# Performance work log

Measured on AMD Instinct MI355X. Metric: run time of the kernel, lower is better.

Reference implementation:

```python
import jax, jax.numpy as jnp
import numpy as np
import math

N, T, D = 4096, 32, 158
NEWS, DGRU = 1024, 128
G, E, H, K = 8, 8, 4, 2          # groups, experts/group, heads, top_k
HID = G * E                       # 64
DH = E // H                       # head_dim = 2
NEG = -1e30


def setup_inputs() -> dict:
    key = jax.random.key(0)
    ks = jax.random.split(key, 16)
    s = 0.05
    price_feature = jax.random.normal(ks[0], (N, T, D), jnp.float32)
    news_feature = jax.random.normal(ks[1], (N, T, NEWS), jnp.float32)
    news_mask = jax.random.uniform(ks[2], (N, T), dtype=jnp.float32)
    # simple deterministic router params (stand-in for injected router module)
    router_W = jax.random.normal(ks[3], (D + NEWS, DGRU), jnp.float32) * s
    router_b = jnp.zeros((DGRU,), jnp.float32)
    # hidden_to_gate: Linear(d_gru -> hidden_dim)
    gate_W = jax.random.normal(ks[4], (DGRU, HID), jnp.float32) * s
    gate_b = jnp.zeros((HID,), jnp.float32)
    # 64 tiny experts: Linear(hidden_dim -> 1), stacked [G,E,HID]
    expert_W = jax.random.normal(ks[5], (G, E, HID), jnp.float32) * s
    expert_b = jnp.zeros((G, E), jnp.float32)
    # per-group attention weights, torch Linear layout [out,in] -> [G,E,E]
    wq = jax.random.normal(ks[6], (G, E, E), jnp.float32) * s
    wk = jax.random.normal(ks[7], (G, E, E), jnp.float32) * s
    wv = jax.random.normal(ks[8], (G, E, E), jnp.float32) * s
    wo = jax.random.normal(ks[9], (G, E, E), jnp.float32) * s
    wq_b = jnp.zeros((G, E), jnp.float32)
    wk_b = jnp.zeros((G, E), jnp.float32)
    wv_b = jnp.zeros((G, E), jnp.float32)
    wo_b = jnp.zeros((G, E), jnp.float32)
    return dict(price_feature=price_feature, news_feature=news_feature, news_mask=news_mask,
                router_W=router_W, router_b=router_b, gate_W=gate_W, gate_b=gate_b,
                expert_W=expert_W, expert_b=expert_b,
                wq=wq, wq_b=wq_b, wk=wk, wk_b=wk_b, wv=wv, wv_b=wv_b, wo=wo, wo_b=wo_b)


def _forward(price_feature, news_feature, news_mask, router_W, router_b,
             gate_W, gate_b, expert_W, expert_b,
             wq, wq_b, wk, wk_b, wv, wv_b, wo, wo_b):
    n = price_feature.shape[0]
    # ---- router: masked temporal pooling + linear + tanh -> [N, d_gru]
    m = news_mask[:, :, None]
    news_agg = (news_feature * m).sum(1) / jnp.clip(m.sum(1), 1e-6)
    price_agg = price_feature.mean(1)
    h = jnp.tanh(jnp.concatenate([price_agg, news_agg], axis=-1) @ router_W + router_b)
    # ---- gate: [N, HID]
    hidden = h @ gate_W + gate_b
    # ---- top-k routing with scatter mask + masked softmax
    top_k_values, top_k_indices = jax.lax.top_k(hidden, K)
    mask = jnp.zeros_like(hidden).at[jnp.arange(n)[:, None], top_k_indices].set(1.0)
    masked_hidden = jnp.where(mask == 0, NEG, hidden)
    routing_weights = jax.nn.softmax(masked_hidden, axis=1)  # [N, HID]
    # ---- all 64 experts at once: [N, G, E]
    expert_out = jnp.einsum('nh,geh->nge', hidden, expert_W) + expert_b
    # ---- inner-group attention (faithful to torch view/transpose layout)
    q = jnp.einsum('nge,gfe->ngf', expert_out, wq) + wq_b
    k = jnp.einsum('nge,gfe->ngf', expert_out, wk) + wk_b
    v = jnp.einsum('nge,gfe->ngf', expert_out, wv) + wv_b
    # view [N,G,H,DH] then transpose(1,2) -> attend over DH positions, H as features
    qt = q.reshape(n, G, H, DH).transpose(0, 1, 3, 2)  # [N,G,DH,H]
    kt = k.reshape(n, G, H, DH).transpose(0, 1, 3, 2)
    vt = v.reshape(n, G, H, DH).transpose(0, 1, 3, 2)
    scores = jnp.einsum('ngdh,ngeh->ngde', qt, kt) / math.sqrt(DH)  # [N,G,DH,DH]
    attn = jax.nn.softmax(scores, axis=-1)
    attended = jnp.einsum('ngde,ngeh->ngdh', attn, vt)  # [N,G,DH,H]
    attended = attended.transpose(0, 1, 3, 2).reshape(n, G, E)
    agg = jnp.einsum('nge,gfe->ngf', attended, wo) + wo_b  # [N,G,E]
    all_outputs = agg.reshape(n, HID)
    weighted = all_outputs * routing_weights
    predictions = weighted.sum(axis=1)  # [N]
    return predictions, routing_weights, hidden, top_k_indices, routing_weights


def reference(price_feature, news_feature, news_mask, router_W, router_b,
              gate_W, gate_b, expert_W, expert_b,
              wq, wq_b, wk, wk_b, wv, wv_b, wo, wo_b):
    return _forward(price_feature, news_feature, news_mask, router_W, router_b,
                    gate_W, gate_b, expert_W, expert_b,
                    wq, wq_b, wk, wk_b, wv, wv_b, wo, wo_b)
```

## Files before the change

kernel.cpp:

```cpp
#include <hip/hip_runtime.h>
#include <math.h>

namespace {

constexpr int TT    = 32;
constexpr int DD    = 158;
constexpr int NEWSC = 1024;
constexpr int XPAD  = 1184;
constexpr int NOFF  = 160;
constexpr int DGRU  = 128;
constexpr int HIDN  = 64;
constexpr int RPB   = 8;

__global__ __launch_bounds__(256)
void agg_kernel(const float* __restrict__ price,
                const float* __restrict__ news,
                const float* __restrict__ mask,
                float* __restrict__ x)
{
  const int r   = blockIdx.x;
  const int tid = threadIdx.x;
  __shared__ float m_s[TT];

  if (tid < TT) m_s[tid] = mask[(size_t)r * TT + tid];
  __syncthreads();

  float den = 0.f;
  #pragma unroll
  for (int t = 0; t < TT; ++t) den += m_s[t];
  den = fmaxf(den, 1e-6f);
  const float rden = 1.0f / den;

  {
    const int j0 = tid * 4;
    const float* nb = news + (size_t)r * TT * NEWSC + j0;
    float ax = 0.f, ay = 0.f, az = 0.f, aw = 0.f;
    #pragma unroll
    for (int t = 0; t < TT; ++t) {
      const float  mv = m_s[t];
      const float4 nv = *(const float4*)(nb + (size_t)t * NEWSC);
      ax += mv * nv.x; ay += mv * nv.y; az += mv * nv.z; aw += mv * nv.w;
    }
    float4 o4 = make_float4(ax * rden, ay * rden, az * rden, aw * rden);
    *(float4*)(x + (size_t)r * XPAD + NOFF + j0) = o4;
  }

  if (tid < DD) {
    const float* pr = price + (size_t)r * TT * DD + tid;
    float acc = 0.f;
    #pragma unroll
    for (int t = 0; t < TT; ++t) acc += pr[(size_t)t * DD];
    x[(size_t)r * XPAD + tid] = acc * (1.0f / (float)TT);
  }
}

__global__ __launch_bounds__(256)
void moe_kernel(const float* __restrict__ x,
                const float* __restrict__ rW,
                const float* __restrict__ rb,
                const float* __restrict__ gW,
                const float* __restrict__ gb,
                const float* __restrict__ eW,
                const float* __restrict__ eb,
                const float* __restrict__ wq,
                const float* __restrict__ wqb,
                const float* __restrict__ wk,
                const float* __restrict__ wkb,
                const float* __restrict__ wv,
                const float* __restrict__ wvb,
                const float* __restrict__ wo,
                const float* __restrict__ wob,
                float* __restrict__ out, int nrows)
{
  __shared__ float hs[RPB][DGRU];
  __shared__ float part[RPB][DGRU];
  __shared__ float hid_s[RPB][HIDN];
  __shared__ float eo_s[RPB][HIDN];
  __shared__ float q_s[RPB][HIDN];
  __shared__ float k_s[RPB][HIDN];
  __shared__ float v_s[RPB][HIDN];
  __shared__ float att_s[RPB][HIDN];

  const int tid  = threadIdx.x;
  const int row0 = blockIdx.x * RPB;

  {
    const int sh = tid >> 7;
    const int o  = tid & 127;
    float acc[RPB];
    #pragma unroll
    for (int r = 0; r < RPB; ++r) acc[r] = 0.f;

    const float* xb = x + (size_t)row0 * XPAD;

    auto seg = [&](int b, int e, int xbase, int wbase) {
      int i = b;
      for (; i + 8 <= e; i += 8) {
        float w[8];
        #pragma unroll
        for (int kk = 0; kk < 8; ++kk)
          w[kk] = rW[(size_t)(wbase + i + kk) * DGRU + o];
        #pragma unroll
        for (int r = 0; r < RPB; ++r) {
          const float* xr = xb + (size_t)r * XPAD + xbase + i;
          acc[r] += xr[0] * w[0] + xr[1] * w[1] + xr[2] * w[2] + xr[3] * w[3]
                  + xr[4] * w[4] + xr[5] * w[5] + xr[6] * w[6] + xr[7] * w[7];
        }
      }
      for (; i < e; ++i) {
        const float w = rW[(size_t)(wbase + i) * DGRU + o];
        #pragma unroll
        for (int r = 0; r < RPB; ++r)
          acc[r] += xb[(size_t)r * XPAD + xbase + i] * w;
      }
    };

    if (!sh) {
      seg(0, 80, 0, 0);
      seg(0, 512, NOFF, DD);
    } else {
      seg(80, DD, 0, 0);
      seg(512, NEWSC, NOFF, DD);
    }

    if (sh) {
      #pragma unroll
      for (int r = 0; r < RPB; ++r) part[r][o] = acc[r];
    }
    __syncthreads();
    if (!sh) {
      const float b = rb[o];
      #pragma unroll
      for (int r = 0; r < RPB; ++r) hs[r][o] = tanhf(acc[r] + part[r][o] + b);
    }
  }
  __syncthreads();

  const int wgi = tid >> 6;
  const int ln  = tid & 63;
  const int ra  = wgi;
  const int rb2 = wgi + 4;

  float h0 = gb[ln], h1 = gb[ln];
  #pragma unroll 4
  for (int i = 0; i < DGRU; ++i) {
    const float w = gW[(size_t)i * HIDN + ln];
    h0 += hs[ra][i]  * w;
    h1 += hs[rb2][i] * w;
  }
  hid_s[ra][ln]  = h0;
  hid_s[rb2][ln] = h1;
  __syncthreads();

  float* out_pred = out;
  float* out_rw1  = out + (size_t)nrows;
  float* out_hid  = out + (size_t)nrows * 65;
  float* out_idx  = out + (size_t)nrows * 129;
  float* out_rw2  = out + (size_t)nrows * 131;

  const float hvv[2] = {h0, h1};
  int   i1v[2], i2v[2];
  float w1v[2], w2v[2];
  #pragma unroll
  for (int rr = 0; rr < 2; ++rr) {
    const int r   = wgi + rr * 4;
    const int row = row0 + r;
    const float hv = hvv[rr];
    float bv = hv; int bi = ln;
    #pragma unroll
    for (int off = 32; off >= 1; off >>= 1) {
      const float ov = __shfl_xor(bv, off);
      const int   oi = __shfl_xor(bi, off);
      if (ov > bv || (ov == bv && oi < bi)) { bv = ov; bi = oi; }
    }
    float cv = (ln == bi) ? -1e30f : hv; int ci = ln;
    #pragma unroll
    for (int off = 32; off >= 1; off >>= 1) {
      const float ov = __shfl_xor(cv, off);
      const int   oi = __shfl_xor(ci, off);
      if (ov > cv || (ov == cv && oi < ci)) { cv = ov; ci = oi; }
    }
    const float e2 = expf(cv - bv);
    const float zi = 1.0f / (1.0f + e2);
    const float rwl = (ln == bi) ? zi : (ln == ci) ? e2 * zi : 0.0f;
    out_hid[(size_t)row * 64 + ln] = hv;
    out_rw1[(size_t)row * 64 + ln] = rwl;
    out_rw2[(size_t)row * 64 + ln] = rwl;
    if (ln < 2) out_idx[(size_t)row * 2 + ln] = (float)(ln == 0 ? bi : ci);
    i1v[rr] = bi; i2v[rr] = ci; w1v[rr] = zi; w2v[rr] = e2 * zi;
  }

  {
    float a0 = eb[ln], a1 = eb[ln];
    const float4* ew4 = (const float4*)(eW + (size_t)ln * HIDN);
    #pragma unroll
    for (int c = 0; c < 16; ++c) {
      const float4 w4 = ew4[c];
      const int j = c * 4;
      a0 += hid_s[ra][j]  * w4.x + hid_s[ra][j+1]  * w4.y
          + hid_s[ra][j+2]  * w4.z + hid_s[ra][j+3]  * w4.w;
      a1 += hid_s[rb2][j] * w4.x + hid_s[rb2][j+1] * w4.y
          + hid_s[rb2][j+2] * w4.z + hid_s[rb2][j+3] * w4.w;
    }
    eo_s[ra][ln]  = a0;
    eo_s[rb2][ln] = a1;
  }
  __syncthreads();

  const int gg = ln >> 3;
  #pragma unroll
  for (int rr = 0; rr < 2; ++rr) {
    const int r = wgi + rr * 4;
    float aq = wqb[ln], ak = wkb[ln], av = wvb[ln];
    #pragma unroll
    for (int ee = 0; ee < 8; ++ee) {
      const float xv = eo_s[r][gg * 8 + ee];
      aq += xv * wq[ln * 8 + ee];
      ak += xv * wk[ln * 8 + ee];
      av += xv * wv[ln * 8 + ee];
    }
    q_s[r][ln] = aq; k_s[r][ln] = ak; v_s[r][ln] = av;
  }
  __syncthreads();

  {
    const int e8  = ln & 7;
    const int dd2 = e8 & 1;
    const int hh  = e8 >> 1;
    const float rs2 = 0.7071067811865476f;
    #pragma unroll
    for (int rr = 0; rr < 2; ++rr) {
      const int r = wgi + rr * 4;
      float s0 = 0.f, s1 = 0.f;
      #pragma unroll
      for (int h2 = 0; h2 < 4; ++h2) {
        const float qv = q_s[r][gg * 8 + h2 * 2 + dd2];
        s0 += qv * k_s[r][gg * 8 + h2 * 2 + 0];
        s1 += qv * k_s[r][gg * 8 + h2 * 2 + 1];
      }
      s0 *= rs2; s1 *= rs2;
      const float mx = fmaxf(s0, s1);
      const float a0 = expf(s0 - mx);
      const float a1 = expf(s1 - mx);
      const float zi = 1.0f / (a0 + a1);
      att_s[r][ln] = (a0 * v_s[r][gg * 8 + hh * 2 + 0]
                    + a1 * v_s[r][gg * 8 + hh * 2 + 1]) * zi;
    }
  }
  __syncthreads();

  #pragma unroll
  for (int rr = 0; rr < 2; ++rr) {
    const int r   = wgi + rr * 4;
    const int row = row0 + r;
    float acc = wob[ln];
    #pragma unroll
    for (int ee = 0; ee < 8; ++ee)
      acc += att_s[r][gg * 8 + ee] * wo[ln * 8 + ee];
    const float rwl = (ln == i1v[rr]) ? w1v[rr] : (ln == i2v[rr]) ? w2v[rr] : 0.0f;
    float ps = acc * rwl;
    #pragma unroll
    for (int off = 32; off >= 1; off >>= 1) ps += __shfl_xor(ps, off);
    if (ln == 0) out_pred[row] = ps;
  }
}

}

extern "C" void kernel_launch(void* const* d_in, const int* in_sizes, int n_in,
                              void* d_out, int out_size, void* d_ws, size_t ws_size,
                              hipStream_t stream) {
  const float* price = (const float*)d_in[0];
  const float* news  = (const float*)d_in[1];
  const float* mask  = (const float*)d_in[2];
  const float* rW    = (const float*)d_in[3];
  const float* rb    = (const float*)d_in[4];
  const float* gW    = (const float*)d_in[5];
  const float* gb    = (const float*)d_in[6];
  const float* eW    = (const float*)d_in[7];
  const float* eb    = (const float*)d_in[8];
  const float* wq    = (const float*)d_in[9];
  const float* wqb   = (const float*)d_in[10];
  const float* wk    = (const float*)d_in[11];
  const float* wkb   = (const float*)d_in[12];
  const float* wv    = (const float*)d_in[13];
  const float* wvb   = (const float*)d_in[14];
  const float* wo    = (const float*)d_in[15];
  const float* wob   = (const float*)d_in[16];
  float* out = (float*)d_out;
  float* xws = (float*)d_ws;
  const int nrows = in_sizes[2] / TT;
  (void)out_size; (void)n_in; (void)ws_size;

  agg_kernel<<<dim3(nrows), dim3(256), 0, stream>>>(price, news, mask, xws);
  moe_kernel<<<dim3(nrows / RPB), dim3(256), 0, stream>>>(
      xws, rW, rb, gW, gb, eW, eb,
      wq, wqb, wk, wkb, wv, wvb, wo, wob, out, nrows);
}
```

Measured before the change: 835.2 us.

## Fuse temporal aggregation into MoE kernel and keep per-row math in registers

Merges the masked pooling kernel into the MoE kernel so pooled features are built in shared memory instead of a global workspace. Rows per block drop from 8 to 4, with one wavefront per row, and the gate, expert, attention and output stages use wavefront shuffles instead of shared arrays and block barriers. This removes a launch and the workspace round trip. In exchange, router weight reuse per block is halved and each thread has less load parallelism during aggregation.

```diff
diff --git a/kernel.cpp b/kernel.cpp
--- a/kernel.cpp
+++ b/kernel.cpp
@@ -6,56 +6,16 @@
 constexpr int TT    = 32;
 constexpr int DD    = 158;
 constexpr int NEWSC = 1024;
-constexpr int XPAD  = 1184;
 constexpr int NOFF  = 160;
+constexpr int XP    = 1184;
 constexpr int DGRU  = 128;
 constexpr int HIDN  = 64;
-constexpr int RPB   = 8;
+constexpr int RPB   = 4;
 
 __global__ __launch_bounds__(256)
-void agg_kernel(const float* __restrict__ price,
+void miga_fused(const float* __restrict__ price,
                 const float* __restrict__ news,
                 const float* __restrict__ mask,
-                float* __restrict__ x)
-{
-  const int r   = blockIdx.x;
-  const int tid = threadIdx.x;
-  __shared__ float m_s[TT];
-
-  if (tid < TT) m_s[tid] = mask[(size_t)r * TT + tid];
-  __syncthreads();
-
-  float den = 0.f;
-  #pragma unroll
-  for (int t = 0; t < TT; ++t) den += m_s[t];
-  den = fmaxf(den, 1e-6f);
-  const float rden = 1.0f / den;
-
-  {
-    const int j0 = tid * 4;
-    const float* nb = news + (size_t)r * TT * NEWSC + j0;
-    float ax = 0.f, ay = 0.f, az = 0.f, aw = 0.f;
-    #pragma unroll
-    for (int t = 0; t < TT; ++t) {
-      const float  mv = m_s[t];
-      const float4 nv = *(const float4*)(nb + (size_t)t * NEWSC);
-      ax += mv * nv.x; ay += mv * nv.y; az += mv * nv.z; aw += mv * nv.w;
-    }
-    float4 o4 = make_float4(ax * rden, ay * rden, az * rden, aw * rden);
-    *(float4*)(x + (size_t)r * XPAD + NOFF + j0) = o4;
-  }
-
-  if (tid < DD) {
-    const float* pr = price + (size_t)r * TT * DD + tid;
-    float acc = 0.f;
-    #pragma unroll
-    for (int t = 0; t < TT; ++t) acc += pr[(size_t)t * DD];
-    x[(size_t)r * XPAD + tid] = acc * (1.0f / (float)TT);
-  }
-}
-
-__global__ __launch_bounds__(256)
-void moe_kernel(const float* __restrict__ x,
                 const float* __restrict__ rW,
                 const float* __restrict__ rb,
                 const float* __restrict__ gW,
@@ -72,17 +32,52 @@
                 const float* __restrict__ wob,
                 float* __restrict__ out, int nrows)
 {
+  __shared__ __align__(16) float xs[RPB][XP];
+  __shared__ float m_s[RPB][TT];
+  __shared__ float part[RPB][DGRU];
   __shared__ float hs[RPB][DGRU];
-  __shared__ float part[RPB][DGRU];
-  __shared__ float hid_s[RPB][HIDN];
-  __shared__ float eo_s[RPB][HIDN];
-  __shared__ float q_s[RPB][HIDN];
-  __shared__ float k_s[RPB][HIDN];
-  __shared__ float v_s[RPB][HIDN];
-  __shared__ float att_s[RPB][HIDN];
 
   const int tid  = threadIdx.x;
   const int row0 = blockIdx.x * RPB;
+
+  if (tid < RPB * TT) {
+    const int r = tid >> 5, t = tid & 31;
+    m_s[r][t] = mask[(size_t)(row0 + r) * TT + t];
+  }
+  __syncthreads();
+
+  if (tid < DD) {
+    #pragma unroll
+    for (int r = 0; r < RPB; ++r) {
+      const float* pr = price + (size_t)(row0 + r) * TT * DD + tid;
+      float acc = 0.f;
+      #pragma unroll 8
+      for (int t = 0; t < TT; ++t) acc += pr[(size_t)t * DD];
+      xs[r][tid] = acc * (1.0f / 32.0f);
+    }
+  }
+
+  {
+    const int j0 = tid * 4;
+    #pragma unroll
+    for (int r = 0; r < RPB; ++r) {
+      float den = 0.f;
+      #pragma unroll
+      for (int t = 0; t < TT; ++t) den += m_s[r][t];
+      const float rden = 1.0f / fmaxf(den, 1e-6f);
+      const float* nb = news + (size_t)(row0 + r) * TT * NEWSC + j0;
+      float ax = 0.f, ay = 0.f, az = 0.f, aw = 0.f;
+      #pragma unroll 8
+      for (int t = 0; t < TT; ++t) {
+        const float  mv = m_s[r][t];
+        const float4 nv = *(const float4*)(nb + (size_t)t * NEWSC);
+        ax += mv * nv.x; ay += mv * nv.y; az += mv * nv.z; aw += mv * nv.w;
+      }
+      *(float4*)(&xs[r][NOFF + j0]) =
+          make_float4(ax * rden, ay * rden, az * rden, aw * rden);
+    }
+  }
+  __syncthreads();
 
   {
     const int sh = tid >> 7;
@@ -90,8 +85,6 @@
     float acc[RPB];
     #pragma unroll
     for (int r = 0; r < RPB; ++r) acc[r] = 0.f;
-
-    const float* xb = x + (size_t)row0 * XPAD;
 
     auto seg = [&](int b, int e, int xbase, int wbase) {
       int i = b;
@@ -102,26 +95,21 @@
           w[kk] = rW[(size_t)(wbase + i + kk) * DGRU + o];
         #pragma unroll
         for (int r = 0; r < RPB; ++r) {
-          const float* xr = xb + (size_t)r * XPAD + xbase + i;
-          acc[r] += xr[0] * w[0] + xr[1] * w[1] + xr[2] * w[2] + xr[3] * w[3]
-                  + xr[4] * w[4] + xr[5] * w[5] + xr[6] * w[6] + xr[7] * w[7];
+          const float4 xa = *(const float4*)&xs[r][xbase + i];
+          const float4 xb = *(const float4*)&xs[r][xbase + i + 4];
+          acc[r] += xa.x * w[0] + xa.y * w[1] + xa.z * w[2] + xa.w * w[3]
+                  + xb.x * w[4] + xb.y * w[5] + xb.z * w[6] + xb.w * w[7];
         }
       }
       for (; i < e; ++i) {
         const float w = rW[(size_t)(wbase + i) * DGRU + o];
         #pragma unroll
-        for (int r = 0; r < RPB; ++r)
-          acc[r] += xb[(size_t)r * XPAD + xbase + i] * w;
+        for (int r = 0; r < RPB; ++r) acc[r] += xs[r][xbase + i] * w;
       }
     };
 
-    if (!sh) {
-      seg(0, 80, 0, 0);
-      seg(0, 512, NOFF, DD);
-    } else {
-      seg(80, DD, 0, 0);
-      seg(512, NEWSC, NOFF, DD);
-    }
+    if (!sh) { seg(0, 80, 0, 0);   seg(0, 512, NOFF, DD); }
+    else     { seg(80, DD, 0, 0);  seg(512, NEWSC, NOFF, DD); }
 
     if (sh) {
       #pragma unroll
@@ -136,21 +124,14 @@
   }
   __syncthreads();
 
-  const int wgi = tid >> 6;
+  const int wvi = tid >> 6;
   const int ln  = tid & 63;
-  const int ra  = wgi;
-  const int rb2 = wgi + 4;
-
-  float h0 = gb[ln], h1 = gb[ln];
+  const int row = row0 + wvi;
+
+  float hid = gb[ln];
   #pragma unroll 4
-  for (int i = 0; i < DGRU; ++i) {
-    const float w = gW[(size_t)i * HIDN + ln];
-    h0 += hs[ra][i]  * w;
-    h1 += hs[rb2][i] * w;
-  }
-  hid_s[ra][ln]  = h0;
-  hid_s[rb2][ln] = h1;
-  __syncthreads();
+  for (int i = 0; i < DGRU; ++i)
+    hid += hs[wvi][i] * gW[(size_t)i * HIDN + ln];
 
   float* out_pred = out;
   float* out_rw1  = out + (size_t)nrows;
@@ -158,111 +139,76 @@
   float* out_idx  = out + (size_t)nrows * 129;
   float* out_rw2  = out + (size_t)nrows * 131;
 
-  const float hvv[2] = {h0, h1};
-  int   i1v[2], i2v[2];
-  float w1v[2], w2v[2];
-  #pragma unroll
-  for (int rr = 0; rr < 2; ++rr) {
-    const int r   = wgi + rr * 4;
-    const int row = row0 + r;
-    const float hv = hvv[rr];
-    float bv = hv; int bi = ln;
-    #pragma unroll
-    for (int off = 32; off >= 1; off >>= 1) {
-      const float ov = __shfl_xor(bv, off);
-      const int   oi = __shfl_xor(bi, off);
-      if (ov > bv || (ov == bv && oi < bi)) { bv = ov; bi = oi; }
-    }
-    float cv = (ln == bi) ? -1e30f : hv; int ci = ln;
-    #pragma unroll
-    for (int off = 32; off >= 1; off >>= 1) {
-      const float ov = __shfl_xor(cv, off);
-      const int   oi = __shfl_xor(ci, off);
-      if (ov > cv || (ov == cv && oi < ci)) { cv = ov; ci = oi; }
-    }
-    const float e2 = expf(cv - bv);
-    const float zi = 1.0f / (1.0f + e2);
-    const float rwl = (ln == bi) ? zi : (ln == ci) ? e2 * zi : 0.0f;
-    out_hid[(size_t)row * 64 + ln] = hv;
-    out_rw1[(size_t)row * 64 + ln] = rwl;
-    out_rw2[(size_t)row * 64 + ln] = rwl;
-    if (ln < 2) out_idx[(size_t)row * 2 + ln] = (float)(ln == 0 ? bi : ci);
-    i1v[rr] = bi; i2v[rr] = ci; w1v[rr] = zi; w2v[rr] = e2 * zi;
-  }
-
+  float bv = hid; int bi = ln;
+  #pragma unroll
+  for (int off = 32; off >= 1; off >>= 1) {
+    const float ov = __shfl_xor(bv, off);
+    const int   oi = __shfl_xor(bi, off);
+    if (ov > bv || (ov == bv && oi < bi)) { bv = ov; bi = oi; }
+  }
+  float cv = (ln == bi) ? -1e30f : hid; int ci = ln;
+  #pragma unroll
+  for (int off = 32; off >= 1; off >>= 1) {
+    const float ov = __shfl_xor(cv, off);
+    const int   oi = __shfl_xor(ci, off);
+    if (ov > cv || (ov == cv && oi < ci)) { cv = ov; ci = oi; }
+  }
+  const float e2 = expf(cv - bv);
+  const float zi = 1.0f / (1.0f + e2);
+  const float rwl = (ln == bi) ? zi : (ln == ci) ? e2 * zi : 0.0f;
+  out_hid[(size_t)row * 64 + ln] = hid;
+  out_rw1[(size_t)row * 64 + ln] = rwl;
+  out_rw2[(size_t)row * 64 + ln] = rwl;
+  if (ln < 2) out_idx[(size_t)row * 2 + ln] = (float)(ln == 0 ? bi : ci);
+
+  float eo = eb[ln];
   {
-    float a0 = eb[ln], a1 = eb[ln];
     const float4* ew4 = (const float4*)(eW + (size_t)ln * HIDN);
     #pragma unroll
     for (int c = 0; c < 16; ++c) {
       const float4 w4 = ew4[c];
-      const int j = c * 4;
-      a0 += hid_s[ra][j]  * w4.x + hid_s[ra][j+1]  * w4.y
-          + hid_s[ra][j+2]  * w4.z + hid_s[ra][j+3]  * w4.w;
-      a1 += hid_s[rb2][j] * w4.x + hid_s[rb2][j+1] * w4.y
-          + hid_s[rb2][j+2] * w4.z + hid_s[rb2][j+3] * w4.w;
-    }
-    eo_s[ra][ln]  = a0;
-    eo_s[rb2][ln] = a1;
-  }
-  __syncthreads();
+      eo += __shfl(hid, c * 4 + 0) * w4.x + __shfl(hid, c * 4 + 1) * w4.y
+          + __shfl(hid, c * 4 + 2) * w4.z + __shfl(hid, c * 4 + 3) * w4.w;
+    }
+  }
 
   const int gg = ln >> 3;
-  #pragma unroll
-  for (int rr = 0; rr < 2; ++rr) {
-    const int r = wgi + rr * 4;
-    float aq = wqb[ln], ak = wkb[ln], av = wvb[ln];
-    #pragma unroll
-    for (int ee = 0; ee < 8; ++ee) {
-      const float xv = eo_s[r][gg * 8 + ee];
-      aq += xv * wq[ln * 8 + ee];
-      ak += xv * wk[ln * 8 + ee];
-      av += xv * wv[ln * 8 + ee];
-    }
-    q_s[r][ln] = aq; k_s[r][ln] = ak; v_s[r][ln] = av;
-  }
-  __syncthreads();
-
-  {
-    const int e8  = ln & 7;
-    const int dd2 = e8 & 1;
-    const int hh  = e8 >> 1;
-    const float rs2 = 0.7071067811865476f;
-    #pragma unroll
-    for (int rr = 0; rr < 2; ++rr) {
-      const int r = wgi + rr * 4;
-      float s0 = 0.f, s1 = 0.f;
-      #pragma unroll
-      for (int h2 = 0; h2 < 4; ++h2) {
-        const float qv = q_s[r][gg * 8 + h2 * 2 + dd2];
-        s0 += qv * k_s[r][gg * 8 + h2 * 2 + 0];
-        s1 += qv * k_s[r][gg * 8 + h2 * 2 + 1];
-      }
-      s0 *= rs2; s1 *= rs2;
-      const float mx = fmaxf(s0, s1);
-      const float a0 = expf(s0 - mx);
-      const float a1 = expf(s1 - mx);
-      const float zi = 1.0f / (a0 + a1);
-      att_s[r][ln] = (a0 * v_s[r][gg * 8 + hh * 2 + 0]
-                    + a1 * v_s[r][gg * 8 + hh * 2 + 1]) * zi;
-    }
-  }
-  __syncthreads();
-
-  #pragma unroll
-  for (int rr = 0; rr < 2; ++rr) {
-    const int r   = wgi + rr * 4;
-    const int row = row0 + r;
-    float acc = wob[ln];
-    #pragma unroll
-    for (int ee = 0; ee < 8; ++ee)
-      acc += att_s[r][gg * 8 + ee] * wo[ln * 8 + ee];
-    const float rwl = (ln == i1v[rr]) ? w1v[rr] : (ln == i2v[rr]) ? w2v[rr] : 0.0f;
-    float ps = acc * rwl;
-    #pragma unroll
-    for (int off = 32; off >= 1; off >>= 1) ps += __shfl_xor(ps, off);
-    if (ln == 0) out_pred[row] = ps;
-  }
+  float aq = wqb[ln], ak = wkb[ln], av = wvb[ln];
+  #pragma unroll
+  for (int ee = 0; ee < 8; ++ee) {
+    const float xv = __shfl(eo, gg * 8 + ee);
+    aq += xv * wq[ln * 8 + ee];
+    ak += xv * wk[ln * 8 + ee];
+    av += xv * wv[ln * 8 + ee];
+  }
+
+  const int e8  = ln & 7;
+  const int dd2 = e8 & 1;
+  const int hh  = e8 >> 1;
+  float s0 = 0.f, s1 = 0.f;
+  #pragma unroll
+  for (int h2 = 0; h2 < 4; ++h2) {
+    const float qv = __shfl(aq, gg * 8 + h2 * 2 + dd2);
+    s0 += qv * __shfl(ak, gg * 8 + h2 * 2 + 0);
+    s1 += qv * __shfl(ak, gg * 8 + h2 * 2 + 1);
+  }
+  const float rs2 = 0.7071067811865476f;
+  s0 *= rs2; s1 *= rs2;
+  const float mx = fmaxf(s0, s1);
+  const float a0 = expf(s0 - mx);
+  const float a1 = expf(s1 - mx);
+  const float ziA = 1.0f / (a0 + a1);
+  const float att = (a0 * __shfl(av, gg * 8 + hh * 2 + 0)
+                   + a1 * __shfl(av, gg * 8 + hh * 2 + 1)) * ziA;
+
+  float acc = wob[ln];
+  #pragma unroll
+  for (int ee = 0; ee < 8; ++ee)
+    acc += __shfl(att, gg * 8 + ee) * wo[ln * 8 + ee];
+  float ps = acc * rwl;
+  #pragma unroll
+  for (int off = 32; off >= 1; off >>= 1) ps += __shfl_xor(ps, off);
+  if (ln == 0) out_pred[row] = ps;
 }
 
 }
@@ -288,12 +234,9 @@
   const float* wo    = (const float*)d_in[15];
   const float* wob   = (const float*)d_in[16];
   float* out = (float*)d_out;
-  float* xws = (float*)d_ws;
   const int nrows = in_sizes[2] / TT;
-  (void)out_size; (void)n_in; (void)ws_size;
-
-  agg_kernel<<<dim3(nrows), dim3(256), 0, stream>>>(price, news, mask, xws);
-  moe_kernel<<<dim3(nrows / RPB), dim3(256), 0, stream>>>(
-      xws, rW, rb, gW, gb, eW, eb,
+  (void)d_ws; (void)ws_size; (void)out_size; (void)n_in;
+  miga_fused<<<dim3(nrows / RPB), dim3(256), 0, stream>>>(
+      price, news, mask, rW, rb, gW, gb, eW, eb,
       wq, wqb, wk, wkb, wv, wvb, wo, wob, out, nrows);
 }
```

Result: faster. 817.9 us (-2.1%).
